# Optimization experiments

Measured on AMD Instinct MI355X. Metric: run time of the kernel, lower is better.

Reference implementation:

```python
import jax, jax.numpy as jnp
import numpy as np

NUM_HEADS = 8
H_NUM, W_NUM = 1, 2   # idx=0 stripe windows
SCALE = float((256 // NUM_HEADS) ** -0.5)  # qk_scale


def _partition(x, h_sp, w_sp):
    # x: (T,B,C,H,W) -> (T, B*nWin, heads, N, C//heads) with N = h_sp*w_sp
    T, B, C, H, W = x.shape
    x = x.reshape(T, B, C, H // h_sp, h_sp, W // w_sp, w_sp)
    x = x.transpose(0, 1, 3, 5, 4, 6, 2)  # T,B,nH,nW,h_sp,w_sp,C
    x = x.reshape(T, -1, h_sp * w_sp, NUM_HEADS, C // NUM_HEADS)
    return x.transpose(0, 1, 3, 2, 4)


def setup_inputs() -> dict:
    key = jax.random.key(0)
    k1, k2, k3 = jax.random.split(key, 3)
    shape = (4, 2, 256, 56, 56)
    return {
        "q": jax.random.normal(k1, shape, jnp.float32),
        "k": jax.random.normal(k2, shape, jnp.float32),
        "v": jax.random.normal(k3, shape, jnp.float32),
        "v_lamda": 1,
    }


def reference(q, k, v, v_lamda):
    T, B, C, H0, W0 = q.shape
    h_pad = (-H0) % H_NUM
    w_pad = (-W0) % W_NUM
    pad = ((0, 0), (0, 0), (0, 0), (0, h_pad), (0, w_pad))
    q = jnp.pad(q, pad)
    k = jnp.pad(k, pad)
    v = jnp.pad(v, pad)
    H, W = H0 + h_pad, W0 + w_pad
    h_sp, w_sp = H // H_NUM, W // W_NUM

    qw = _partition(q, h_sp, w_sp)  # (T, BnW, h, N, d)
    kw = _partition(k, h_sp, w_sp)
    vw = _partition(v, h_sp, w_sp)  # head dim = C*v_lamda//heads

    attn = jnp.einsum('twhnd,twhmd->twhnm', qw, kw)          # (QK^T), no softmax
    out = jnp.einsum('twhnm,twhmd->twhnd', attn, vw) * (SCALE * 2)

    # merge windows back: (T,BnW,h,N,d) -> (T,B,Cv,H,W)
    Cv = C * v_lamda
    out = out.transpose(0, 1, 3, 2, 4).reshape(T, -1, h_sp * w_sp, Cv)
    out = out.reshape(T, B, H_NUM, W_NUM, h_sp, w_sp, Cv)
    out = out.transpose(0, 1, 2, 4, 3, 5, 6).reshape(T, B, H, W, Cv)
    out = out.transpose(0, 1, 4, 2, 3)
    return out[:, :, :, :H0, :W0]
```

## Files before the change

kernel.cpp:

```cpp
#include <hip/hip_runtime.h>


#define HW 3136
#define WDIM 56
#define NPOS 1568
#define NPROB 128
#define SPLIT 14
#define PSPLIT 112
#define LROW 36
#define SCALE2 0.35355339059327373f

__global__ __launch_bounds__(256) void kv_kernel(const float* __restrict__ K,
                                                 const float* __restrict__ V,
                                                 float* __restrict__ Mpart) {
    __shared__ float lds[2 * PSPLIT * LROW];
    float* kT = lds;
    float* vT = lds + PSPLIT * LROW;

    const int blk = blockIdx.x;
    const int p   = blk / SPLIT;
    const int s   = blk - p * SPLIT;
    const int head = p & 7;
    const int win  = (p >> 3) & 1;
    const int b    = (p >> 4) & 1;
    const int t    = p >> 5;

    const size_t base = (size_t)((t * 2 + b) * 256 + head * 32) * HW;
    const float* __restrict__ Kb = K + base;
    const float* __restrict__ Vb = V + base;

    const int tid = threadIdx.x;

    #pragma unroll
    for (int j = 0; j < 7; ++j) {
        const int item = tid + 256 * j;
        const int isv  = item >= 896 ? 1 : 0;
        const int r    = item - isv * 896;
        const int chg  = r / 112;
        const int pp   = r - chg * 112;
        const int n  = s * PSPLIT + pp;
        const int y  = n / 28;
        const int x  = n - y * 28;
        const float* src = (isv ? Vb : Kb)
                         + (size_t)chg * 4 * HW + y * WDIM + win * 28 + x;
        float4 val;
        val.x = src[0];
        val.y = src[HW];
        val.z = src[2 * HW];
        val.w = src[3 * HW];
        float* dst = isv ? vT : kT;
        *(float4*)&dst[pp * LROW + chg * 4] = val;
    }
    __syncthreads();

    const int l   = tid & 63;
    const int w   = tid >> 6;
    const int dd0 = (l >> 3) * 4;
    const int de0 = (l & 7) * 4;

    float acc[4][4] = {{0.f}};
    const int p0 = w * 28;
    #pragma unroll 4
    for (int pp = p0; pp < p0 + 28; ++pp) {
        const float4 ka = *(const float4*)&kT[pp * LROW + dd0];
        const float4 va = *(const float4*)&vT[pp * LROW + de0];
        acc[0][0] += ka.x * va.x; acc[0][1] += ka.x * va.y;
        acc[0][2] += ka.x * va.z; acc[0][3] += ka.x * va.w;
        acc[1][0] += ka.y * va.x; acc[1][1] += ka.y * va.y;
        acc[1][2] += ka.y * va.z; acc[1][3] += ka.y * va.w;
        acc[2][0] += ka.z * va.x; acc[2][1] += ka.z * va.y;
        acc[2][2] += ka.z * va.z; acc[2][3] += ka.z * va.w;
        acc[3][0] += ka.w * va.x; acc[3][1] += ka.w * va.y;
        acc[3][2] += ka.w * va.z; acc[3][3] += ka.w * va.w;
    }
    __syncthreads();

    #pragma unroll
    for (int i = 0; i < 4; ++i)
        #pragma unroll
        for (int jj = 0; jj < 4; ++jj)
            lds[w * 1024 + (dd0 + i) * 32 + (de0 + jj)] = acc[i][jj];
    __syncthreads();

    const float4 r0 = *(const float4*)&lds[tid * 4];
    const float4 r1 = *(const float4*)&lds[1024 + tid * 4];
    const float4 r2 = *(const float4*)&lds[2048 + tid * 4];
    const float4 r3 = *(const float4*)&lds[3072 + tid * 4];
    float4 o;
    o.x = r0.x + r1.x + r2.x + r3.x;
    o.y = r0.y + r1.y + r2.y + r3.y;
    o.z = r0.z + r1.z + r2.z + r3.z;
    o.w = r0.w + r1.w + r2.w + r3.w;
    *(float4*)&Mpart[(size_t)blk * 1024 + tid * 4] = o;
}

__global__ __launch_bounds__(256) void qm_kernel(const float* __restrict__ Q,
                                                 const float* __restrict__ Mpart,
                                                 float* __restrict__ Out) {
    __shared__ float M[1024];
    const int blk = blockIdx.x;
    const int p   = blk / 7;
    const int c   = blk - p * 7;
    const int tid = threadIdx.x;

    const float* mp = Mpart + (size_t)p * SPLIT * 1024 + tid * 4;
    float4 sum = {0.f, 0.f, 0.f, 0.f};
    #pragma unroll
    for (int s = 0; s < SPLIT; ++s) {
        const float4 v = *(const float4*)&mp[s * 1024];
        sum.x += v.x; sum.y += v.y; sum.z += v.z; sum.w += v.w;
    }
    sum.x *= SCALE2; sum.y *= SCALE2; sum.z *= SCALE2; sum.w *= SCALE2;
    *(float4*)&M[tid * 4] = sum;
    __syncthreads();

    const int head = p & 7;
    const int win  = (p >> 3) & 1;
    const int b    = (p >> 4) & 1;
    const int t    = p >> 5;

    if (tid < 224) {
        const int n = c * 224 + tid;
        const int y = n / 28;
        const int x = n - y * 28;
        const size_t base = (size_t)((t * 2 + b) * 256 + head * 32) * HW
                          + y * WDIM + win * 28 + x;
        const float* __restrict__ Qb = Q + base;
        float* __restrict__ Ob = Out + base;

        float acc[32] = {0.f};
        #pragma unroll 8
        for (int dd = 0; dd < 32; ++dd) {
            const float qv = Qb[(size_t)dd * HW];
            #pragma unroll
            for (int g = 0; g < 8; ++g) {
                const float4 m = *(const float4*)&M[dd * 32 + g * 4];
                acc[g * 4 + 0] += qv * m.x;
                acc[g * 4 + 1] += qv * m.y;
                acc[g * 4 + 2] += qv * m.z;
                acc[g * 4 + 3] += qv * m.w;
            }
        }
        #pragma unroll
        for (int de = 0; de < 32; ++de)
            Ob[(size_t)de * HW] = acc[de];
    }
}

extern "C" void kernel_launch(void* const* d_in, const int* in_sizes, int n_in,
                              void* d_out, int out_size, void* d_ws, size_t ws_size,
                              hipStream_t stream) {
    const float* q = (const float*)d_in[0];
    const float* k = (const float*)d_in[1];
    const float* v = (const float*)d_in[2];
    float* out   = (float*)d_out;
    float* Mpart = (float*)d_ws;

    kv_kernel<<<NPROB * SPLIT, 256, 0, stream>>>(k, v, Mpart);
    qm_kernel<<<NPROB * 7, 256, 0, stream>>>(q, Mpart, out);
}
```

Baseline: 126.6 us.

## Stage K/V tiles via direct global-to-LDS loads and prefetch Q rows

The K/V staging in kv_kernel now uses 16-byte global_load_lds transfers straight into LDS. This removes the register round-trip and the four strided scalar loads per item. The LDS layout becomes channel-major without padding, and the inner product loop is rewritten to read float4 runs along the position axis. In qm_kernel, all 32 Q values per thread are loaded up front so the global loads can be in flight together. The unpadded channel stride of 112 floats may cause LDS bank conflicts on the compute reads, and the extra Q registers raise register pressure.

Result: slower. 135.5 us (+7.0%).

```diff
diff --git a/kernel.cpp b/kernel.cpp
--- a/kernel.cpp
+++ b/kernel.cpp
@@ -7,15 +7,15 @@
 #define NPROB 128
 #define SPLIT 14
 #define PSPLIT 112
-#define LROW 36
 #define SCALE2 0.35355339059327373f
+
+typedef const __attribute__((address_space(1))) void gas_void;
+typedef __attribute__((address_space(3))) void las_void;
 
 __global__ __launch_bounds__(256) void kv_kernel(const float* __restrict__ K,
                                                  const float* __restrict__ V,
                                                  float* __restrict__ Mpart) {
-    __shared__ float lds[2 * PSPLIT * LROW];
-    float* kT = lds;
-    float* vT = lds + PSPLIT * LROW;
+    __shared__ float lds[2 * 32 * PSPLIT];
 
     const int blk = blockIdx.x;
     const int p   = blk / SPLIT;
@@ -30,48 +30,45 @@
     const float* __restrict__ Vb = V + base;
 
     const int tid = threadIdx.x;
+    const int l   = tid & 63;
+    const int w   = tid >> 6;
 
     #pragma unroll
-    for (int j = 0; j < 7; ++j) {
-        const int item = tid + 256 * j;
-        const int isv  = item >= 896 ? 1 : 0;
-        const int r    = item - isv * 896;
-        const int chg  = r / 112;
-        const int pp   = r - chg * 112;
-        const int n  = s * PSPLIT + pp;
-        const int y  = n / 28;
-        const int x  = n - y * 28;
+    for (int i = 0; i < 7; ++i) {
+        const int q   = (w * 7 + i) * 64 + l;
+        const int isv = q >= 896 ? 1 : 0;
+        const int r   = q - isv * 896;
+        const int ch  = r / 28;
+        const int pq  = r - ch * 28;
+        const int n   = s * PSPLIT + pq * 4;
+        const int y   = n / 28;
+        const int x   = n - y * 28;
         const float* src = (isv ? Vb : Kb)
-                         + (size_t)chg * 4 * HW + y * WDIM + win * 28 + x;
-        float4 val;
-        val.x = src[0];
-        val.y = src[HW];
-        val.z = src[2 * HW];
-        val.w = src[3 * HW];
-        float* dst = isv ? vT : kT;
-        *(float4*)&dst[pp * LROW + chg * 4] = val;
+                         + (size_t)ch * HW + y * WDIM + win * 28 + x;
+        float* dst = &lds[w * 1792 + i * 256];
+        __builtin_amdgcn_global_load_lds((gas_void*)src, (las_void*)dst, 16, 0, 0);
     }
     __syncthreads();
 
-    const int l   = tid & 63;
-    const int w   = tid >> 6;
     const int dd0 = (l >> 3) * 4;
     const int de0 = (l & 7) * 4;
 
     float acc[4][4] = {{0.f}};
-    const int p0 = w * 28;
-    #pragma unroll 4
-    for (int pp = p0; pp < p0 + 28; ++pp) {
-        const float4 ka = *(const float4*)&kT[pp * LROW + dd0];
-        const float4 va = *(const float4*)&vT[pp * LROW + de0];
-        acc[0][0] += ka.x * va.x; acc[0][1] += ka.x * va.y;
-        acc[0][2] += ka.x * va.z; acc[0][3] += ka.x * va.w;
-        acc[1][0] += ka.y * va.x; acc[1][1] += ka.y * va.y;
-        acc[1][2] += ka.y * va.z; acc[1][3] += ka.y * va.w;
-        acc[2][0] += ka.z * va.x; acc[2][1] += ka.z * va.y;
-        acc[2][2] += ka.z * va.z; acc[2][3] += ka.z * va.w;
-        acc[3][0] += ka.w * va.x; acc[3][1] += ka.w * va.y;
-        acc[3][2] += ka.w * va.z; acc[3][3] += ka.w * va.w;
+    #pragma unroll
+    for (int j = 0; j < 7; ++j) {
+        const int n0 = 28 * w + 4 * j;
+        float4 ka[4], va[4];
+        #pragma unroll
+        for (int i = 0; i < 4; ++i) {
+            ka[i] = *(const float4*)&lds[(dd0 + i) * PSPLIT + n0];
+            va[i] = *(const float4*)&lds[32 * PSPLIT + (de0 + i) * PSPLIT + n0];
+        }
+        #pragma unroll
+        for (int i = 0; i < 4; ++i)
+            #pragma unroll
+            for (int jj = 0; jj < 4; ++jj)
+                acc[i][jj] += ka[i].x * va[jj].x + ka[i].y * va[jj].y
+                            + ka[i].z * va[jj].z + ka[i].w * va[jj].w;
     }
     __syncthreads();
 
@@ -128,17 +125,21 @@
         const float* __restrict__ Qb = Q + base;
         float* __restrict__ Ob = Out + base;
 
+        float qv[32];
+        #pragma unroll
+        for (int dd = 0; dd < 32; ++dd)
+            qv[dd] = Qb[(size_t)dd * HW];
+
         float acc[32] = {0.f};
         #pragma unroll 8
         for (int dd = 0; dd < 32; ++dd) {
-            const float qv = Qb[(size_t)dd * HW];
             #pragma unroll
             for (int g = 0; g < 8; ++g) {
                 const float4 m = *(const float4*)&M[dd * 32 + g * 4];
-                acc[g * 4 + 0] += qv * m.x;
-                acc[g * 4 + 1] += qv * m.y;
-                acc[g * 4 + 2] += qv * m.z;
-                acc[g * 4 + 3] += qv * m.w;
+                acc[g * 4 + 0] += qv[dd] * m.x;
+                acc[g * 4 + 1] += qv[dd] * m.y;
+                acc[g * 4 + 2] += qv[dd] * m.z;
+                acc[g * 4 + 3] += qv[dd] * m.w;
             }
         }
         #pragma unroll
```
